# Performance work log

Hardware: AMD Instinct MI355X
Metric: run time of the kernel (lower is better)

Reference implementation:

```python
import jax, jax.numpy as jnp
import numpy as np
import math

D_MODEL = 1024
D_K = 256
B, T = 4, 4096

def setup_inputs() -> dict:
    key = jax.random.key(0)
    ks = jax.random.split(key, 7)
    s = 1.0 / math.sqrt(D_MODEL)
    return {
        "inputs": jax.random.normal(ks[0], (B, T, D_MODEL), dtype=jnp.float32),
        "Wq": jax.random.uniform(ks[1], (D_MODEL, D_K), jnp.float32, -s, s),
        "bq": jax.random.uniform(ks[2], (D_K,), jnp.float32, -s, s),
        "Wk": jax.random.uniform(ks[3], (D_MODEL, D_K), jnp.float32, -s, s),
        "bk": jax.random.uniform(ks[4], (D_K,), jnp.float32, -s, s),
        "Wv": jax.random.uniform(ks[5], (D_MODEL, D_K), jnp.float32, -s, s),
        "bv": jax.random.uniform(ks[6], (D_K,), jnp.float32, -s, s),
    }

def reference(inputs, Wq, bq, Wk, bk, Wv, bv):
    q = inputs @ Wq + bq                      # [B,T,d_k]
    k = inputs @ Wk + bk
    v = inputs @ Wv + bv
    scores = jnp.einsum('btd,bsd->bts', q, k)  # [B,T,T]
    Tdim = inputs.shape[1]
    causal = jnp.tril(jnp.ones((Tdim, Tdim), dtype=bool))
    # faithful to original: mask with -1e9 BEFORE dividing by sqrt(d_k)
    scores = jnp.where(causal[None], scores, jnp.float32(-1e9))
    attn = jax.nn.softmax(scores / math.sqrt(D_K), axis=-1)
    return jnp.einsum('bts,bsd->btd', attn, v)
```

## Files before the change

kernel.cpp:

```cpp
#include <hip/hip_runtime.h>
#include <stdint.h>

typedef uint16_t u16;
typedef uint32_t u32;
typedef float    f32x4  __attribute__((ext_vector_type(4)));
typedef short    bf16x8 __attribute__((ext_vector_type(8)));
typedef u32      u32x4  __attribute__((ext_vector_type(4)));
typedef u16      u16x8  __attribute__((ext_vector_type(8)));
typedef u16      u16x4  __attribute__((ext_vector_type(4)));

#define MFMA16(a, b, c) __builtin_amdgcn_mfma_f32_16x16x32_bf16((a), (b), (c), 0, 0, 0)


__device__ __forceinline__ u16 f2bf(float f) {
  u32 x = __float_as_uint(f);
  return (u16)((x + 0x7FFFu + ((x >> 16) & 1u)) >> 16);
}

__global__ __launch_bounds__(256) void cvt_x_kernel(const float* __restrict__ X,
                                                    u16* __restrict__ Xb) {
  int i = (blockIdx.x * 256 + threadIdx.x) * 8;
  f32x4 a = *(const f32x4*)(X + i);
  f32x4 b = *(const f32x4*)(X + i + 4);
  u16x8 o;
  o[0] = f2bf(a[0]); o[1] = f2bf(a[1]); o[2] = f2bf(a[2]); o[3] = f2bf(a[3]);
  o[4] = f2bf(b[0]); o[5] = f2bf(b[1]); o[6] = f2bf(b[2]); o[7] = f2bf(b[3]);
  *(u16x8*)(Xb + i) = o;
}

__global__ __launch_bounds__(256) void cvt_w_kernel(const float* __restrict__ Wq,
                                                    const float* __restrict__ Wk,
                                                    const float* __restrict__ Wv,
                                                    u16* __restrict__ Wt) {
  int idx = blockIdx.x * 256 + threadIdx.x;
  int m = idx >> 18;
  int n = (idx >> 10) & 255;
  int k = idx & 1023;
  const float* W = (m == 0) ? Wq : (m == 1) ? Wk : Wv;
  Wt[idx] = f2bf(W[k * 256 + n]);
}

__global__ __launch_bounds__(256) void qkv_gemm_kernel(
    const u16* __restrict__ Xb, const u16* __restrict__ Wt,
    const float* __restrict__ bq, const float* __restrict__ bk, const float* __restrict__ bv,
    u16* __restrict__ Qb, u16* __restrict__ Kb, u16* __restrict__ Vtb) {
  __shared__ __align__(16) char sm[32768];
  const int tid = threadIdx.x;
  const int wid = tid >> 6, lane = tid & 63, g = lane >> 4, lr = lane & 15;
  const int wr = wid >> 1, wc = wid & 1;
  const int m0 = blockIdx.x * 128, n0 = blockIdx.y * 128, z = blockIdx.z;
  const u16* W = Wt + z * 262144;

  f32x4 acc[4][4];
#pragma unroll
  for (int mi = 0; mi < 4; ++mi)
#pragma unroll
    for (int ni = 0; ni < 4; ++ni) {
      acc[mi][ni][0] = 0.f; acc[mi][ni][1] = 0.f; acc[mi][ni][2] = 0.f; acc[mi][ni][3] = 0.f;
    }

  for (int k0 = 0; k0 < 1024; k0 += 64) {
    __syncthreads();
#pragma unroll
    for (int r = 0; r < 4; ++r) {
      int ch = r * 256 + tid;
      int row = ch >> 3, c = ch & 7;
      u32x4 vx = *(const u32x4*)(Xb + (size_t)(m0 + row) * 1024 + k0 + c * 8);
      *(u32x4*)(sm + row * 128 + 16 * (c ^ (row & 7))) = vx;
      u32x4 vw = *(const u32x4*)(W + (size_t)(n0 + row) * 1024 + k0 + c * 8);
      *(u32x4*)(sm + 16384 + row * 128 + 16 * (c ^ (row & 7))) = vw;
    }
    __syncthreads();
#pragma unroll
    for (int kk = 0; kk < 2; ++kk) {
      bf16x8 af[4], bfr[4];
#pragma unroll
      for (int mi = 0; mi < 4; ++mi) {
        int row = wr * 64 + mi * 16 + lr;
        af[mi] = *(const bf16x8*)(sm + row * 128 + 16 * ((kk * 4 + g) ^ (row & 7)));
      }
#pragma unroll
      for (int ni = 0; ni < 4; ++ni) {
        int row = wc * 64 + ni * 16 + lr;
        bfr[ni] = *(const bf16x8*)(sm + 16384 + row * 128 + 16 * ((kk * 4 + g) ^ (row & 7)));
      }
#pragma unroll
      for (int mi = 0; mi < 4; ++mi)
#pragma unroll
        for (int ni = 0; ni < 4; ++ni)
          acc[mi][ni] = MFMA16(af[mi], bfr[ni], acc[mi][ni]);
    }
  }

  const float* bias = (z == 0) ? bq : (z == 1) ? bk : bv;
  if (z < 2) {
    u16* O = (z == 0) ? Qb : Kb;
    const float qscale = (z == 0) ? 0.0625f : 1.0f;
#pragma unroll
    for (int ni = 0; ni < 4; ++ni) {
      int col = n0 + wc * 64 + ni * 16 + lr;
      float bb = bias[col];
#pragma unroll
      for (int mi = 0; mi < 4; ++mi)
#pragma unroll
        for (int j = 0; j < 4; ++j) {
          int row = m0 + wr * 64 + mi * 16 + 4 * g + j;
          O[(size_t)row * 256 + col] = f2bf((acc[mi][ni][j] + bb) * qscale);
        }
    }
  } else {
    __syncthreads();
#pragma unroll
    for (int ni = 0; ni < 4; ++ni) {
      int cl = wc * 64 + ni * 16 + lr;
      float bb = bias[n0 + cl];
#pragma unroll
      for (int mi = 0; mi < 4; ++mi)
#pragma unroll
        for (int j = 0; j < 4; ++j) {
          int rl = wr * 64 + mi * 16 + 4 * g + j;
          *(u16*)(sm + cl * 256 + rl * 2) = f2bf(acc[mi][ni][j] + bb);
        }
    }
    __syncthreads();
    int bidx = m0 >> 12, tb = m0 & 4095;
#pragma unroll
    for (int r = 0; r < 8; ++r) {
      int ch = r * 256 + tid;
      int cl = ch >> 4, tp = ch & 15;
      u32x4 v = *(const u32x4*)(sm + cl * 256 + tp * 16);
      *(u32x4*)(Vtb + (size_t)bidx * 1048576 + (size_t)(n0 + cl) * 4096 + tb + tp * 8) = v;
    }
  }
}

__global__ __launch_bounds__(256) void flash_kernel(
    const u16* __restrict__ Qb, const u16* __restrict__ Kb,
    const u16* __restrict__ Vtb, u16* __restrict__ Opart, float2* __restrict__ ML,
    int s, int gx) {
  __shared__ __align__(16) char sm[36864];
  const int tid = threadIdx.x, wid = tid >> 6, lane = tid & 63, g = lane >> 4, lr = lane & 15;
  const int b = blockIdx.y;
  const int G = 64 >> s;
  int x = blockIdx.x, g4 = 0;
  while (g4 < G - 1 && x >= (((g4 + 1) * (g4 + 2)) << (s - 1))) ++g4;
  const int local = x - ((g4 * (g4 + 1)) << (s - 1));
  const int qq = local / (g4 + 1);
  const int sc = local - qq * (g4 + 1);
  const int qb = (g4 << s) + qq;
  const int t0 = qb * 64;
  const int w0 = t0 + wid * 16;
  const int C = 64 << s;
  const int sbase = sc * C;

  bf16x8 qf[8];
  const u16* Qrow = Qb + (size_t)(b * 4096 + w0 + lr) * 256;
#pragma unroll
  for (int kk = 0; kk < 8; ++kk) qf[kk] = *(const bf16x8*)(Qrow + kk * 32 + g * 8);

  f32x4 o[16];
#pragma unroll
  for (int n = 0; n < 16; ++n) { o[n][0] = 0.f; o[n][1] = 0.f; o[n][2] = 0.f; o[n][3] = 0.f; }
  float m_ = -1e30f, l_ = 0.f;

  const int nt = min(C >> 5, (t0 + 64 - sbase) >> 5);
  for (int st = 0; st < nt; ++st) {
    const int s0 = sbase + st * 32;
    __syncthreads();
#pragma unroll
    for (int r = 0; r < 4; ++r) {
      int ch = r * 256 + tid;
      {
        int srow = ch >> 5, c = ch & 31;
        u32x4 v = *(const u32x4*)(Kb + (size_t)(b * 4096 + s0 + srow) * 256 + c * 8);
        *(u32x4*)(sm + srow * 512 + 16 * (c ^ (srow & 7))) = v;
      }
      {
        int d = ch >> 2, c = ch & 3;
        u32x4 v = *(const u32x4*)(Vtb + (size_t)b * 1048576 + (size_t)d * 4096 + s0 + c * 8);
        *(u32x4*)(sm + 16384 + d * 64 + 16 * (c ^ ((d >> 1) & 3))) = v;
      }
    }
    __syncthreads();

    if (s0 <= w0 + 15) {
      f32x4 sa[2];
#pragma unroll
      for (int ni = 0; ni < 2; ++ni) { sa[ni][0] = 0.f; sa[ni][1] = 0.f; sa[ni][2] = 0.f; sa[ni][3] = 0.f; }
#pragma unroll
      for (int ni = 0; ni < 2; ++ni) {
        int srw = ni * 16 + lr;
#pragma unroll
        for (int kk = 0; kk < 8; ++kk) {
          bf16x8 kf = *(const bf16x8*)(sm + srw * 512 + 16 * ((kk * 4 + g) ^ (srw & 7)));
          sa[ni] = MFMA16(kf, qf[kk], sa[ni]);
        }
      }
      const int t = w0 + lr;
      if (s0 + 31 > w0) {
#pragma unroll
        for (int ni = 0; ni < 2; ++ni)
#pragma unroll
          for (int j = 0; j < 4; ++j) {
            int ss = s0 + ni * 16 + 4 * g + j;
            if (t < ss) sa[ni][j] = -1e30f;
          }
      }
      float mt = fmaxf(fmaxf(fmaxf(sa[0][0], sa[0][1]), fmaxf(sa[0][2], sa[0][3])),
                       fmaxf(fmaxf(sa[1][0], sa[1][1]), fmaxf(sa[1][2], sa[1][3])));
      mt = fmaxf(mt, __shfl_xor(mt, 16, 64));
      mt = fmaxf(mt, __shfl_xor(mt, 32, 64));
      float mn = fmaxf(m_, mt);
      float scale = __expf(m_ - mn);
      m_ = mn;
#pragma unroll
      for (int ni = 0; ni < 2; ++ni)
#pragma unroll
        for (int j = 0; j < 4; ++j) sa[ni][j] = __expf(sa[ni][j] - m_);
      float su = (sa[0][0] + sa[0][1]) + (sa[0][2] + sa[0][3]) +
                 (sa[1][0] + sa[1][1]) + (sa[1][2] + sa[1][3]);
      su += __shfl_xor(su, 16, 64);
      su += __shfl_xor(su, 32, 64);
      l_ = l_ * scale + su;
#pragma unroll
      for (int n = 0; n < 16; ++n)
#pragma unroll
        for (int j = 0; j < 4; ++j) o[n][j] *= scale;
#pragma unroll
      for (int ni = 0; ni < 2; ++ni)
#pragma unroll
        for (int j = 0; j < 4; ++j) {
          int c = ni * 2 + (g >> 1);
          *(u16*)(sm + 32768 + wid * 1024 + lr * 64 + 16 * (c ^ (lr & 3)) + (4 * (g & 1) + j) * 2) =
              f2bf(sa[ni][j]);
        }
      asm volatile("s_waitcnt lgkmcnt(0)" ::: "memory");
      bf16x8 pf = *(const bf16x8*)(sm + 32768 + wid * 1024 + lr * 64 + 16 * (g ^ (lr & 3)));
#pragma unroll
      for (int n = 0; n < 16; ++n) {
        int d = n * 16 + lr;
        bf16x8 vf = *(const bf16x8*)(sm + 16384 + d * 64 + 16 * (g ^ ((d >> 1) & 3)));
        o[n] = MFMA16(vf, pf, o[n]);
      }
    }
  }

  u16* Orow = Opart + ((size_t)(b * gx + blockIdx.x) * 64 + wid * 16) * 256;
#pragma unroll
  for (int n = 0; n < 16; ++n) {
    u16x4 pk;
    pk[0] = f2bf(o[n][0]); pk[1] = f2bf(o[n][1]); pk[2] = f2bf(o[n][2]); pk[3] = f2bf(o[n][3]);
    *(u16x4*)(Orow + lr * 256 + n * 16 + 4 * g) = pk;
  }
  if (lane < 16) {
    float2 ml; ml.x = m_; ml.y = l_;
    ML[(size_t)(b * gx + blockIdx.x) * 64 + wid * 16 + lane] = ml;
  }
}

__global__ __launch_bounds__(256) void combine_kernel(const u16* __restrict__ Opart,
                                                      const float2* __restrict__ ML,
                                                      float* __restrict__ out,
                                                      int s, int gx) {
  const int wid = threadIdx.x >> 6, lane = threadIdx.x & 63;
  const int rg = blockIdx.x * 4 + wid;
  const int b = rg >> 12, t = rg & 4095;
  const int qb = t >> 6;
  const int gg = qb >> s, qq = qb & ((1 << s) - 1);
  const int n = gg + 1;
  const size_t base = (size_t)(b * gx) + ((gg * (gg + 1)) << (s - 1)) + qq * (gg + 1);
  const int tl = t & 63;
  float mv[16], lv[16], w[16];
  float M = -1e30f;
#pragma unroll
  for (int sc = 0; sc < 16; ++sc)
    if (sc < n) {
      float2 ml = ML[(base + sc) * 64 + tl];
      mv[sc] = ml.x; lv[sc] = ml.y;
      M = fmaxf(M, ml.x);
    }
  float L = 0.f;
#pragma unroll
  for (int sc = 0; sc < 16; ++sc)
    if (sc < n) { w[sc] = __expf(mv[sc] - M); L += w[sc] * lv[sc]; }
  const float inv = 1.0f / L;
  const int c0 = lane * 4;
  float a0 = 0.f, a1 = 0.f, a2 = 0.f, a3 = 0.f;
#pragma unroll
  for (int sc = 0; sc < 16; ++sc)
    if (sc < n) {
      u16x4 v = *(const u16x4*)(Opart + ((base + sc) * 64 + tl) * 256 + c0);
      a0 += w[sc] * __uint_as_float((u32)v[0] << 16);
      a1 += w[sc] * __uint_as_float((u32)v[1] << 16);
      a2 += w[sc] * __uint_as_float((u32)v[2] << 16);
      a3 += w[sc] * __uint_as_float((u32)v[3] << 16);
    }
  f32x4 r; r[0] = a0 * inv; r[1] = a1 * inv; r[2] = a2 * inv; r[3] = a3 * inv;
  *(f32x4*)(out + (size_t)rg * 256 + c0) = r;
}

extern "C" void kernel_launch(void* const* d_in, const int* in_sizes, int n_in,
                              void* d_out, int out_size, void* d_ws, size_t ws_size,
                              hipStream_t stream) {
  const float* X  = (const float*)d_in[0];
  const float* Wq = (const float*)d_in[1];
  const float* bq = (const float*)d_in[2];
  const float* Wk = (const float*)d_in[3];
  const float* bk = (const float*)d_in[4];
  const float* Wv = (const float*)d_in[5];
  const float* bv = (const float*)d_in[6];
  float* out = (float*)d_out;
  char* ws = (char*)d_ws;

  const size_t OFF_WT  = 33554432;
  const size_t OFF_Q   = OFF_WT + 1572864;
  const size_t OFF_K   = OFF_Q + 8388608;
  const size_t OFF_VT  = OFF_K + 8388608;
  const size_t PREFIX  = OFF_VT + 8388608;

  const size_t NEEDED_A = PREFIX + 589824 + 37748736;
  const size_t NEEDED_B = PREFIX + 327680;
  if (ws_size < NEEDED_B) return;

  u16* Xb  = (u16*)ws;
  u16* Wt  = (u16*)(ws + OFF_WT);
  u16* Qb  = (u16*)(ws + OFF_Q);
  u16* Kb  = (u16*)(ws + OFF_K);
  u16* Vtb = (u16*)(ws + OFF_VT);

  int s, gx;
  u16* Opart;
  float2* ML;
  if (ws_size >= NEEDED_A) {
    s = 3; gx = 288;
    ML = (float2*)(ws + PREFIX);
    Opart = (u16*)(ws + PREFIX + 589824);
  } else {
    s = 4; gx = 160;
    ML = (float2*)(ws + PREFIX);
    Opart = (u16*)ws;
  }

  cvt_x_kernel<<<8192, 256, 0, stream>>>(X, Xb);
  cvt_w_kernel<<<3072, 256, 0, stream>>>(Wq, Wk, Wv, Wt);
  qkv_gemm_kernel<<<dim3(128, 2, 3), 256, 0, stream>>>(Xb, Wt, bq, bk, bv, Qb, Kb, Vtb);
  flash_kernel<<<dim3(gx, 4), 256, 0, stream>>>(Qb, Kb, Vtb, Opart, ML, s, gx);
  combine_kernel<<<4096, 256, 0, stream>>>(Opart, ML, out, s, gx);
}
```

Before: 178.7 us.

## Prefetch next K/V tile into registers, lazy rescale, shuffle-based P transpose

The flash kernel now loads the next K/V tile from global memory into registers while the current tile is computed, so global latency overlaps with the MFMA work. The online-softmax rescale of the accumulator is skipped unless some row's max grows by more than 8, which avoids 64 multiplies per tile in most iterations. The P tile is repacked into MFMA operand layout with cross-lane shuffles instead of a round trip through shared memory, which drops the P scratch area and its LDS wait. The trade-offs are higher register pressure from the prefetch buffers, more shuffle instructions, and exponentials that can reach up to e^8 before a rescale, which costs some numerical headroom in bf16.

```diff
diff --git a/kernel.cpp b/kernel.cpp
--- a/kernel.cpp
+++ b/kernel.cpp
@@ -138,7 +138,7 @@
     const u16* __restrict__ Qb, const u16* __restrict__ Kb,
     const u16* __restrict__ Vtb, u16* __restrict__ Opart, float2* __restrict__ ML,
     int s, int gx) {
-  __shared__ __align__(16) char sm[36864];
+  __shared__ __align__(16) char sm[32768];
   const int tid = threadIdx.x, wid = tid >> 6, lane = tid & 63, g = lane >> 4, lr = lane & 15;
   const int b = blockIdx.y;
   const int G = 64 >> s;
@@ -163,24 +163,38 @@
   for (int n = 0; n < 16; ++n) { o[n][0] = 0.f; o[n][1] = 0.f; o[n][2] = 0.f; o[n][3] = 0.f; }
   float m_ = -1e30f, l_ = 0.f;
 
+  const u16* Kbase = Kb + (size_t)b * 4096 * 256;
+  const u16* Vbase = Vtb + (size_t)b * 1048576;
+
+  u32x4 pk[4], pv[4];
   const int nt = min(C >> 5, (t0 + 64 - sbase) >> 5);
+
+#define LOADTILE(s0_)                                                                 \
+  {                                                                                   \
+    _Pragma("unroll")                                                                 \
+    for (int r = 0; r < 4; ++r) {                                                     \
+      int ch = r * 256 + tid;                                                         \
+      int srow = ch >> 5, c = ch & 31;                                                \
+      pk[r] = *(const u32x4*)(Kbase + (size_t)((s0_) + srow) * 256 + c * 8);          \
+      int d = ch >> 2, c2 = ch & 3;                                                   \
+      pv[r] = *(const u32x4*)(Vbase + (size_t)d * 4096 + (s0_) + c2 * 8);             \
+    }                                                                                 \
+  }
+
+  LOADTILE(sbase);
+
   for (int st = 0; st < nt; ++st) {
     const int s0 = sbase + st * 32;
     __syncthreads();
 #pragma unroll
     for (int r = 0; r < 4; ++r) {
       int ch = r * 256 + tid;
-      {
-        int srow = ch >> 5, c = ch & 31;
-        u32x4 v = *(const u32x4*)(Kb + (size_t)(b * 4096 + s0 + srow) * 256 + c * 8);
-        *(u32x4*)(sm + srow * 512 + 16 * (c ^ (srow & 7))) = v;
-      }
-      {
-        int d = ch >> 2, c = ch & 3;
-        u32x4 v = *(const u32x4*)(Vtb + (size_t)b * 1048576 + (size_t)d * 4096 + s0 + c * 8);
-        *(u32x4*)(sm + 16384 + d * 64 + 16 * (c ^ ((d >> 1) & 3))) = v;
-      }
-    }
+      int srow = ch >> 5, c = ch & 31;
+      *(u32x4*)(sm + srow * 512 + 16 * (c ^ (srow & 7))) = pk[r];
+      int d = ch >> 2, c2 = ch & 3;
+      *(u32x4*)(sm + 16384 + d * 64 + 16 * (c2 ^ ((d >> 1) & 3))) = pv[r];
+    }
+    if (st + 1 < nt) LOADTILE(s0 + 32);
     __syncthreads();
 
     if (s0 <= w0 + 15) {
@@ -210,9 +224,16 @@
                        fmaxf(fmaxf(sa[1][0], sa[1][1]), fmaxf(sa[1][2], sa[1][3])));
       mt = fmaxf(mt, __shfl_xor(mt, 16, 64));
       mt = fmaxf(mt, __shfl_xor(mt, 32, 64));
-      float mn = fmaxf(m_, mt);
-      float scale = __expf(m_ - mn);
-      m_ = mn;
+      if (__any(mt > m_ + 8.0f)) {
+        float mn = fmaxf(m_, mt);
+        float scale = __expf(m_ - mn);
+        m_ = mn;
+        l_ *= scale;
+#pragma unroll
+        for (int n = 0; n < 16; ++n)
+#pragma unroll
+          for (int j = 0; j < 4; ++j) o[n][j] *= scale;
+      }
 #pragma unroll
       for (int ni = 0; ni < 2; ++ni)
 #pragma unroll
@@ -221,21 +242,20 @@
                  (sa[1][0] + sa[1][1]) + (sa[1][2] + sa[1][3]);
       su += __shfl_xor(su, 16, 64);
       su += __shfl_xor(su, 32, 64);
-      l_ = l_ * scale + su;
-#pragma unroll
-      for (int n = 0; n < 16; ++n)
-#pragma unroll
-        for (int j = 0; j < 4; ++j) o[n][j] *= scale;
-#pragma unroll
-      for (int ni = 0; ni < 2; ++ni)
-#pragma unroll
-        for (int j = 0; j < 4; ++j) {
-          int c = ni * 2 + (g >> 1);
-          *(u16*)(sm + 32768 + wid * 1024 + lr * 64 + 16 * (c ^ (lr & 3)) + (4 * (g & 1) + j) * 2) =
-              f2bf(sa[ni][j]);
-        }
-      asm volatile("s_waitcnt lgkmcnt(0)" ::: "memory");
-      bf16x8 pf = *(const bf16x8*)(sm + 32768 + wid * 1024 + lr * 64 + 16 * (g ^ (lr & 3)));
+      l_ += su;
+      u32 w0p = (u32)f2bf(sa[0][0]) | ((u32)f2bf(sa[0][1]) << 16);
+      u32 w1p = (u32)f2bf(sa[0][2]) | ((u32)f2bf(sa[0][3]) << 16);
+      u32 w2p = (u32)f2bf(sa[1][0]) | ((u32)f2bf(sa[1][1]) << 16);
+      u32 w3p = (u32)f2bf(sa[1][2]) | ((u32)f2bf(sa[1][3]) << 16);
+      const int s_lo = lr + ((g & 1) ? 32 : 0);
+      u32 A0 = __shfl(w0p, s_lo, 64),      A1 = __shfl(w1p, s_lo, 64);
+      u32 A2 = __shfl(w2p, s_lo, 64),      A3 = __shfl(w3p, s_lo, 64);
+      u32 B0 = __shfl(w0p, s_lo + 16, 64), B1 = __shfl(w1p, s_lo + 16, 64);
+      u32 B2 = __shfl(w2p, s_lo + 16, 64), B3 = __shfl(w3p, s_lo + 16, 64);
+      union { u32 u[4]; bf16x8 v; } pu;
+      if (g < 2) { pu.u[0] = A0; pu.u[1] = A1; pu.u[2] = B0; pu.u[3] = B1; }
+      else       { pu.u[0] = A2; pu.u[1] = A3; pu.u[2] = B2; pu.u[3] = B3; }
+      bf16x8 pf = pu.v;
 #pragma unroll
       for (int n = 0; n < 16; ++n) {
         int d = n * 16 + lr;
@@ -244,13 +264,14 @@
       }
     }
   }
+#undef LOADTILE
 
   u16* Orow = Opart + ((size_t)(b * gx + blockIdx.x) * 64 + wid * 16) * 256;
 #pragma unroll
   for (int n = 0; n < 16; ++n) {
-    u16x4 pk;
-    pk[0] = f2bf(o[n][0]); pk[1] = f2bf(o[n][1]); pk[2] = f2bf(o[n][2]); pk[3] = f2bf(o[n][3]);
-    *(u16x4*)(Orow + lr * 256 + n * 16 + 4 * g) = pk;
+    u16x4 pkk;
+    pkk[0] = f2bf(o[n][0]); pkk[1] = f2bf(o[n][1]); pkk[2] = f2bf(o[n][2]); pkk[3] = f2bf(o[n][3]);
+    *(u16x4*)(Orow + lr * 256 + n * 16 + 4 * g) = pkk;
   }
   if (lane < 16) {
     float2 ml; ml.x = m_; ml.y = l_;
```

After: 227.1 us. 1.27x slower.

## Load 64-key K/V tiles per barrier and skip rescale unless max grows

Applied to the files above, without the earlier changes.

Each block now loads 64 keys of K and V into shared memory per barrier pair and processes them as two 32-key halves, halving the number of __syncthreads and load phases. The online softmax also skips rescaling the output accumulator unless the running max grows by more than 8 (a lazy-rescale threshold), which removes 64 multiplies per tile in the common case. Shared memory grows from 36 KB to 68 KB, which may lower occupancy. The lazy threshold lets exponentials reach up to e^8 before a rescale, which is safe in fp32 but alters rounding slightly.

```diff
diff --git a/kernel.cpp b/kernel.cpp
--- a/kernel.cpp
+++ b/kernel.cpp
@@ -138,7 +138,7 @@
     const u16* __restrict__ Qb, const u16* __restrict__ Kb,
     const u16* __restrict__ Vtb, u16* __restrict__ Opart, float2* __restrict__ ML,
     int s, int gx) {
-  __shared__ __align__(16) char sm[36864];
+  __shared__ __align__(16) char sm[69632];
   const int tid = threadIdx.x, wid = tid >> 6, lane = tid & 63, g = lane >> 4, lr = lane & 15;
   const int b = blockIdx.y;
   const int G = 64 >> s;
@@ -163,27 +163,38 @@
   for (int n = 0; n < 16; ++n) { o[n][0] = 0.f; o[n][1] = 0.f; o[n][2] = 0.f; o[n][3] = 0.f; }
   float m_ = -1e30f, l_ = 0.f;
 
-  const int nt = min(C >> 5, (t0 + 64 - sbase) >> 5);
-  for (int st = 0; st < nt; ++st) {
-    const int s0 = sbase + st * 32;
-    __syncthreads();
-#pragma unroll
-    for (int r = 0; r < 4; ++r) {
-      int ch = r * 256 + tid;
-      {
+  const u16* Kbase = Kb + (size_t)b * 4096 * 256;
+  const u16* Vbase = Vtb + (size_t)b * 1048576;
+
+  const int nto = min(C >> 6, (t0 + 64 - sbase) >> 6);
+  for (int ot = 0; ot < nto; ++ot) {
+    const int os0 = sbase + ot * 64;
+    __syncthreads();
+#pragma unroll
+    for (int half = 0; half < 2; ++half) {
+      const int sh = os0 + 32 * half;
+      char* kb = sm + half * 16384;
+      char* vb = sm + 32768 + half * 16384;
+#pragma unroll
+      for (int r = 0; r < 4; ++r) {
+        int ch = r * 256 + tid;
         int srow = ch >> 5, c = ch & 31;
-        u32x4 v = *(const u32x4*)(Kb + (size_t)(b * 4096 + s0 + srow) * 256 + c * 8);
-        *(u32x4*)(sm + srow * 512 + 16 * (c ^ (srow & 7))) = v;
-      }
-      {
-        int d = ch >> 2, c = ch & 3;
-        u32x4 v = *(const u32x4*)(Vtb + (size_t)b * 1048576 + (size_t)d * 4096 + s0 + c * 8);
-        *(u32x4*)(sm + 16384 + d * 64 + 16 * (c ^ ((d >> 1) & 3))) = v;
-      }
-    }
-    __syncthreads();
-
-    if (s0 <= w0 + 15) {
+        u32x4 v = *(const u32x4*)(Kbase + (size_t)(sh + srow) * 256 + c * 8);
+        *(u32x4*)(kb + srow * 512 + 16 * (c ^ (srow & 7))) = v;
+        int d = ch >> 2, c2 = ch & 3;
+        u32x4 v2 = *(const u32x4*)(Vbase + (size_t)d * 4096 + sh + c2 * 8);
+        *(u32x4*)(vb + d * 64 + 16 * (c2 ^ ((d >> 1) & 3))) = v2;
+      }
+    }
+    __syncthreads();
+
+#pragma unroll 1
+    for (int half = 0; half < 2; ++half) {
+      const int s0 = os0 + 32 * half;
+      if (s0 > w0 + 15) break;
+      const char* kb = sm + half * 16384;
+      const char* vb = sm + 32768 + half * 16384;
+
       f32x4 sa[2];
 #pragma unroll
       for (int ni = 0; ni < 2; ++ni) { sa[ni][0] = 0.f; sa[ni][1] = 0.f; sa[ni][2] = 0.f; sa[ni][3] = 0.f; }
@@ -192,7 +203,7 @@
         int srw = ni * 16 + lr;
 #pragma unroll
         for (int kk = 0; kk < 8; ++kk) {
-          bf16x8 kf = *(const bf16x8*)(sm + srw * 512 + 16 * ((kk * 4 + g) ^ (srw & 7)));
+          bf16x8 kf = *(const bf16x8*)(kb + srw * 512 + 16 * ((kk * 4 + g) ^ (srw & 7)));
           sa[ni] = MFMA16(kf, qf[kk], sa[ni]);
         }
       }
@@ -210,9 +221,16 @@
                        fmaxf(fmaxf(sa[1][0], sa[1][1]), fmaxf(sa[1][2], sa[1][3])));
       mt = fmaxf(mt, __shfl_xor(mt, 16, 64));
       mt = fmaxf(mt, __shfl_xor(mt, 32, 64));
-      float mn = fmaxf(m_, mt);
-      float scale = __expf(m_ - mn);
-      m_ = mn;
+      if (__any(mt > m_ + 8.0f)) {
+        float mn = fmaxf(m_, mt);
+        float scale = __expf(m_ - mn);
+        m_ = mn;
+        l_ *= scale;
+#pragma unroll
+        for (int n = 0; n < 16; ++n)
+#pragma unroll
+          for (int j = 0; j < 4; ++j) o[n][j] *= scale;
+      }
 #pragma unroll
       for (int ni = 0; ni < 2; ++ni)
 #pragma unroll
@@ -221,25 +239,21 @@
                  (sa[1][0] + sa[1][1]) + (sa[1][2] + sa[1][3]);
       su += __shfl_xor(su, 16, 64);
       su += __shfl_xor(su, 32, 64);
-      l_ = l_ * scale + su;
-#pragma unroll
-      for (int n = 0; n < 16; ++n)
-#pragma unroll
-        for (int j = 0; j < 4; ++j) o[n][j] *= scale;
+      l_ += su;
 #pragma unroll
       for (int ni = 0; ni < 2; ++ni)
 #pragma unroll
         for (int j = 0; j < 4; ++j) {
           int c = ni * 2 + (g >> 1);
-          *(u16*)(sm + 32768 + wid * 1024 + lr * 64 + 16 * (c ^ (lr & 3)) + (4 * (g & 1) + j) * 2) =
+          *(u16*)(sm + 65536 + wid * 1024 + lr * 64 + 16 * (c ^ (lr & 3)) + (4 * (g & 1) + j) * 2) =
               f2bf(sa[ni][j]);
         }
       asm volatile("s_waitcnt lgkmcnt(0)" ::: "memory");
-      bf16x8 pf = *(const bf16x8*)(sm + 32768 + wid * 1024 + lr * 64 + 16 * (g ^ (lr & 3)));
+      bf16x8 pf = *(const bf16x8*)(sm + 65536 + wid * 1024 + lr * 64 + 16 * (g ^ (lr & 3)));
 #pragma unroll
       for (int n = 0; n < 16; ++n) {
         int d = n * 16 + lr;
-        bf16x8 vf = *(const bf16x8*)(sm + 16384 + d * 64 + 16 * (g ^ ((d >> 1) & 3)));
+        bf16x8 vf = *(const bf16x8*)(vb + d * 64 + 16 * (g ^ ((d >> 1) & 3)));
         o[n] = MFMA16(vf, pf, o[n]);
       }
     }
```

Result: no change. 176.8 us (-1.0%).
